# Performance work log

Measured on AMD Instinct MI355X. Metric: run time of the kernel, lower is better.

The kernel has to match this reference:

```python
import jax, jax.numpy as jnp
import numpy as np


def setup_inputs() -> dict:
    key = jax.random.key(0)
    k0, k1, k2, k3, k4 = jax.random.split(key, 5)
    B, C, H, W = 32, 64, 128, 128
    return {
        "x": jax.random.normal(k0, (B, C, H, W), jnp.float32),
        "w1d": jax.random.normal(k1, (64,), jnp.float32) * 0.1,   # Conv1d(1,1,k=64,s=64) weight
        "b1d": jax.random.normal(k2, (1,), jnp.float32) * 0.1,    # Conv1d bias
        "wdw": jax.random.normal(k3, (C, 1, 9, 9), jnp.float32) * 0.05,  # depthwise Conv2d weight (OIHW, groups=C)
        "bdw": jax.random.normal(k4, (C,), jnp.float32) * 0.05,   # depthwise Conv2d bias
    }


def _cov_linear(x, w1d, b1d):
    # Batched torch.cov over channels, followed by Conv1d(1,1,k=64,stride=64)
    B, C, H, W = x.shape
    f = x.reshape(B, C, H * W)
    f = f - f.mean(axis=-1, keepdims=True)
    cov = jnp.einsum('bcn,bdn->bcd', f, f) / (H * W - 1)  # [B, C, C]
    # Conv1d with kernel=stride=64 on the flattened C*C vector == segmented dot
    seg = cov.reshape(B, (C * C) // 64, 64)               # [B, C, 64] since C == 64
    return seg @ w1d + b1d                                # [B, C]


def reference(x, w1d, b1d, wdw, bdw):
    C = x.shape[1]
    c = _cov_linear(x, w1d, b1d)
    # 9x9 depthwise conv, padding=4 (same spatial size)
    y = jax.lax.conv_general_dilated(
        x, wdw, window_strides=(1, 1), padding=[(4, 4), (4, 4)],
        dimension_numbers=('NCHW', 'OIHW', 'NCHW'), feature_group_count=C)
    y = y + bdw[None, :, None, None]
    c_ = _cov_linear(y, w1d, b1d)
    raise_ch = jax.nn.softmax(c_ - c, axis=1)             # softmax over channel scores
    att = jax.nn.sigmoid(c_ * (1.0 + raise_ch))           # [B, C]
    return y * att[:, :, None, None]
```

## Files before the change

kernel.cpp:

```cpp
#include <hip/hip_runtime.h>

#define NSP 16384
#define CCH 64
#define BATCH 32
#define SPLIT 4
#define CPB (CCH / SPLIT)

#define LW 160
#define LH 40
#define LDSF (LW * LH)
#define NQ (LDSF / 4)
#define NISS 7

__device__ __forceinline__ void gload_lds16(const float* g, float* l) {
    __builtin_amdgcn_global_load_lds(
        (const __attribute__((address_space(1))) void*)g,
        (__attribute__((address_space(3))) void*)l,
        16, 0, 0);
}

__device__ __forceinline__ int swq(int q) { return q ^ ((q >> 3) & 7); }

__device__ __forceinline__ unsigned short f2bf(float f) {
    unsigned u = __float_as_uint(f);
    u += 0x7fffu + ((u >> 16) & 1u);
    return (unsigned short)(u >> 16);
}
__device__ __forceinline__ float bflo(unsigned u) { return __uint_as_float(u << 16); }
__device__ __forceinline__ float bfhi(unsigned u) { return __uint_as_float(u & 0xffff0000u); }

template<int YBF>
__global__ __launch_bounds__(256, 2) void conv_kernel(
    const float* __restrict__ x, const float* __restrict__ wdw,
    const float* __restrict__ bdw, const float* __restrict__ w1d,
    const float* __restrict__ zpad,
    float* __restrict__ yf, unsigned short* __restrict__ yb,
    float* __restrict__ tx_parts, float* __restrict__ ty_parts,
    float* __restrict__ S_x, float* __restrict__ S_y)
{
    const int tile = blockIdx.x;
    const int b    = blockIdx.y;
    const int sp   = blockIdx.z;
    const int tile_ry = tile * 32;
    const int tid = threadIdx.x;
    const int tx = tid & 15, ty = tid >> 4;
    const int c0 = tx * 8, r0 = ty * 2;
    const int cbase = sp * CPB;

    __shared__ float bufs[2][LDSF];

    int soff[NISS]; unsigned okm = 0;
    #pragma unroll
    for (int r = 0; r < NISS; ++r) {
        int q = tid + 256 * r;
        int lrow = q / 40, qcl = q - lrow * 40;
        int gq = swq(qcl);
        int gr = tile_ry - 4 + lrow;
        int gc = gq * 4 - 4;
        soff[r] = gr * 128 + gc;
        if (q < NQ && (unsigned)gr < 128u && gq >= 1 && gq <= 32) okm |= 1u << r;
    }

    int rb[4];
    #pragma unroll
    for (int j = 0; j < 4; ++j) rb[j] = r0 * LW + swq(2 * tx + j) * 4;

    const float* xb = x + (size_t)b * CCH * NSP;

#define STAGE(cc, dst) do {                                               \
        const float* plane_ = xb + (size_t)(cc) * NSP;                    \
        _Pragma("unroll")                                                 \
        for (int r_ = 0; r_ < NISS; ++r_) {                               \
            int q_ = tid + 256 * r_;                                      \
            if (q_ < NQ) {                                                \
                const float* g_ = ((okm >> r_) & 1u) ? plane_ + soff[r_]  \
                                                     : zpad;              \
                gload_lds16(g_, &(dst)[4 * q_]);                          \
            }                                                             \
        }                                                                 \
    } while (0)

    STAGE(cbase, bufs[0]);

    float txa[2][8] = {};
    float tya[2][8] = {};
    __syncthreads();

    for (int k = 0; k < CPB; ++k) {
        const int c = cbase + k;
        if (k + 1 < CPB) STAGE(c + 1, bufs[(k + 1) & 1]);

        const float* cb = bufs[k & 1];
        const float* wc = wdw + c * 81;
        float acc[2][8] = {};
        float cx[2][8];
        #pragma unroll
        for (int ir = 0; ir < 10; ++ir) {
            float4 f0 = *(const float4*)(cb + rb[0] + ir * LW);
            float4 f1 = *(const float4*)(cb + rb[1] + ir * LW);
            float4 f2 = *(const float4*)(cb + rb[2] + ir * LW);
            float4 f3 = *(const float4*)(cb + rb[3] + ir * LW);
            float v[16] = {f0.x, f0.y, f0.z, f0.w, f1.x, f1.y, f1.z, f1.w,
                           f2.x, f2.y, f2.z, f2.w, f3.x, f3.y, f3.z, f3.w};
            if (ir == 4) {
                #pragma unroll
                for (int q = 0; q < 8; ++q) cx[0][q] = v[q + 4];
            }
            if (ir == 5) {
                #pragma unroll
                for (int q = 0; q < 8; ++q) cx[1][q] = v[q + 4];
            }
            #pragma unroll
            for (int o = 0; o < 2; ++o) {
                int tv = ir - o;
                if (tv >= 0 && tv <= 8) {
                    #pragma unroll
                    for (int kx = 0; kx < 9; ++kx) {
                        float w = wc[tv * 9 + kx];
                        #pragma unroll
                        for (int q = 0; q < 8; ++q) acc[o][q] += w * v[kx + q];
                    }
                }
            }
        }

        const float bias = bdw[c];
        const float w1c  = w1d[c];
        float sx = 0.f, sy = 0.f;
        const size_t ybase = (size_t)(b * CCH + c) * NSP + (tile_ry + r0) * 128 + c0;
        #pragma unroll
        for (int o = 0; o < 2; ++o) {
            float yv[8];
            #pragma unroll
            for (int q = 0; q < 8; ++q) {
                yv[q] = acc[o][q] + bias;
                sx += cx[o][q];
                sy += yv[q];
                txa[o][q] += w1c * cx[o][q];
                tya[o][q] += w1c * yv[q];
            }
            if (YBF) {
                uint4 s;
                s.x = (unsigned)f2bf(yv[0]) | ((unsigned)f2bf(yv[1]) << 16);
                s.y = (unsigned)f2bf(yv[2]) | ((unsigned)f2bf(yv[3]) << 16);
                s.z = (unsigned)f2bf(yv[4]) | ((unsigned)f2bf(yv[5]) << 16);
                s.w = (unsigned)f2bf(yv[6]) | ((unsigned)f2bf(yv[7]) << 16);
                *(uint4*)(yb + ybase + o * 128) = s;
            } else {
                *(float4*)(yf + ybase + o * 128) =
                    make_float4(yv[0], yv[1], yv[2], yv[3]);
                *(float4*)(yf + ybase + o * 128 + 4) =
                    make_float4(yv[4], yv[5], yv[6], yv[7]);
            }
        }

        #pragma unroll
        for (int off = 32; off > 0; off >>= 1) {
            sx += __shfl_down(sx, off);
            sy += __shfl_down(sy, off);
        }
        if ((tid & 63) == 0) {
            atomicAdd(&S_x[b * CCH + c], sx);
            atomicAdd(&S_y[b * CCH + c], sy);
        }
        __syncthreads();
    }
#undef STAGE

    const size_t tb = ((size_t)sp * BATCH + b) * NSP + (tile_ry + r0) * 128 + c0;
    float* txp = tx_parts + tb;
    float* typ = ty_parts + tb;
    #pragma unroll
    for (int o = 0; o < 2; ++o) {
        *(float4*)(txp + o * 128)     = make_float4(txa[o][0], txa[o][1], txa[o][2], txa[o][3]);
        *(float4*)(txp + o * 128 + 4) = make_float4(txa[o][4], txa[o][5], txa[o][6], txa[o][7]);
        *(float4*)(typ + o * 128)     = make_float4(tya[o][0], tya[o][1], tya[o][2], tya[o][3]);
        *(float4*)(typ + o * 128 + 4) = make_float4(tya[o][4], tya[o][5], tya[o][6], tya[o][7]);
    }
}

__global__ __launch_bounds__(256) void collapse_kernel(
    const float4* __restrict__ parts, float4* __restrict__ tcoll)
{
    const int i = blockIdx.x * 256 + threadIdx.x;
    const int tsel = i >> 17;
    const int j = i & 131071;
    const float4* p = parts + (size_t)tsel * SPLIT * 131072;
    float4 s = p[j];
    #pragma unroll
    for (int r = 1; r < SPLIT; ++r) {
        float4 a = p[j + (size_t)r * 131072];
        s.x += a.x; s.y += a.y; s.z += a.z; s.w += a.w;
    }
    tcoll[(size_t)tsel * 131072 + j] = s;
}

template<int YBF>
__global__ __launch_bounds__(256) void dot_kernel(
    const float* __restrict__ x, const float* __restrict__ yf,
    const unsigned short* __restrict__ yb,
    const float* __restrict__ t_x, const float* __restrict__ t_y,
    float* __restrict__ dot_x, float* __restrict__ dot_y)
{
    const int bc = blockIdx.x;
    const int b  = bc >> 6;
    const int tid = threadIdx.x;
    const float4* xr  = (const float4*)(x   + (size_t)bc * NSP);
    const float4* txr = (const float4*)(t_x + (size_t)b * NSP);
    const float4* tyr = (const float4*)(t_y + (size_t)b * NSP);
    float dx = 0.f, dy = 0.f;
    if (YBF) {
        const uint4* yr = (const uint4*)(yb + (size_t)bc * NSP);
        for (int i = tid; i < NSP / 8; i += 256) {
            float4 x0 = xr[2 * i], x1 = xr[2 * i + 1];
            float4 t0 = txr[2 * i], t1 = txr[2 * i + 1];
            float4 u0 = tyr[2 * i], u1 = tyr[2 * i + 1];
            uint4 yv = yr[i];
            dx += x0.x * t0.x + x0.y * t0.y + x0.z * t0.z + x0.w * t0.w
                + x1.x * t1.x + x1.y * t1.y + x1.z * t1.z + x1.w * t1.w;
            dy += bflo(yv.x) * u0.x + bfhi(yv.x) * u0.y
                + bflo(yv.y) * u0.z + bfhi(yv.y) * u0.w
                + bflo(yv.z) * u1.x + bfhi(yv.z) * u1.y
                + bflo(yv.w) * u1.z + bfhi(yv.w) * u1.w;
        }
    } else {
        const float4* yr = (const float4*)(yf + (size_t)bc * NSP);
        for (int i = tid; i < NSP / 4; i += 256) {
            float4 xv = xr[i], tv = txr[i];
            float4 yv = yr[i], uv = tyr[i];
            dx += xv.x * tv.x + xv.y * tv.y + xv.z * tv.z + xv.w * tv.w;
            dy += yv.x * uv.x + yv.y * uv.y + yv.z * uv.z + yv.w * uv.w;
        }
    }
    #pragma unroll
    for (int off = 32; off > 0; off >>= 1) {
        dx += __shfl_down(dx, off);
        dy += __shfl_down(dy, off);
    }
    __shared__ float red[8];
    const int wid = tid >> 6;
    if ((tid & 63) == 0) { red[wid * 2] = dx; red[wid * 2 + 1] = dy; }
    __syncthreads();
    if (tid == 0) {
        dot_x[bc] = red[0] + red[2] + red[4] + red[6];
        dot_y[bc] = red[1] + red[3] + red[5] + red[7];
    }
}

__global__ __launch_bounds__(64) void att_kernel(
    const float* __restrict__ S_x, const float* __restrict__ S_y,
    const float* __restrict__ dot_x, const float* __restrict__ dot_y,
    const float* __restrict__ w1d, const float* __restrict__ b1d,
    float* __restrict__ att)
{
    const int b = blockIdx.x;
    const int c = threadIdx.x;
    const float sx = S_x[b * CCH + c];
    const float sy = S_y[b * CCH + c];
    const float w  = w1d[c];
    float tsx = w * sx, tsy = w * sy;
    #pragma unroll
    for (int off = 32; off > 0; off >>= 1) {
        tsx += __shfl_xor(tsx, off);
        tsy += __shfl_xor(tsy, off);
    }
    const float inv_n  = 1.f / 16384.f;
    const float inv_n1 = 1.f / 16383.f;
    const float bb = b1d[0];
    float cxv = (dot_x[b * CCH + c] - sx * inv_n * tsx) * inv_n1 + bb;
    float cyv = (dot_y[b * CCH + c] - sy * inv_n * tsy) * inv_n1 + bb;
    float d = cyv - cxv;
    float m = d;
    #pragma unroll
    for (int off = 32; off > 0; off >>= 1) m = fmaxf(m, __shfl_xor(m, off));
    float e = __expf(d - m);
    float s = e;
    #pragma unroll
    for (int off = 32; off > 0; off >>= 1) s += __shfl_xor(s, off);
    float r = e / s;
    float a = cyv * (1.f + r);
    att[b * CCH + c] = 1.f / (1.f + __expf(-a));
}

template<int YBF>
__global__ __launch_bounds__(256) void scale_kernel(
    const unsigned short* __restrict__ yb, float* __restrict__ out,
    const float* __restrict__ att)
{
    const size_t total8 = (size_t)BATCH * CCH * NSP / 8;
    size_t i = (size_t)blockIdx.x * blockDim.x + threadIdx.x;
    const size_t stride = (size_t)gridDim.x * blockDim.x;
    if (YBF) {
        for (; i < total8; i += stride) {
            uint4 y = ((const uint4*)yb)[i];
            float a = att[(i * 8) >> 14];
            float4 o0 = make_float4(bflo(y.x) * a, bfhi(y.x) * a,
                                    bflo(y.y) * a, bfhi(y.y) * a);
            float4 o1 = make_float4(bflo(y.z) * a, bfhi(y.z) * a,
                                    bflo(y.w) * a, bfhi(y.w) * a);
            ((float4*)out)[2 * i]     = o0;
            ((float4*)out)[2 * i + 1] = o1;
        }
    } else {
        for (; i < total8; i += stride) {
            float a = att[(i * 8) >> 14];
            float4 v0 = ((const float4*)out)[2 * i];
            float4 v1 = ((const float4*)out)[2 * i + 1];
            v0.x *= a; v0.y *= a; v0.z *= a; v0.w *= a;
            v1.x *= a; v1.y *= a; v1.z *= a; v1.w *= a;
            ((float4*)out)[2 * i]     = v0;
            ((float4*)out)[2 * i + 1] = v1;
        }
    }
}

extern "C" void kernel_launch(void* const* d_in, const int* in_sizes, int n_in,
                              void* d_out, int out_size, void* d_ws, size_t ws_size,
                              hipStream_t stream) {
    const float* x   = (const float*)d_in[0];
    const float* w1d = (const float*)d_in[1];
    const float* b1d = (const float*)d_in[2];
    const float* wdw = (const float*)d_in[3];
    const float* bdw = (const float*)d_in[4];
    float* out = (float*)d_out;
    float* fw  = (float*)d_ws;

    const size_t PARTS = (size_t)SPLIT * BATCH * NSP;
    float* tx_parts = fw;
    float* ty_parts = tx_parts + PARTS;
    float* t_x      = ty_parts + PARTS;
    float* t_y      = t_x + (size_t)BATCH * NSP;
    float* S_x      = t_y + (size_t)BATCH * NSP;
    float* S_y      = S_x + 2048;
    float* dot_x    = S_y + 2048;
    float* dot_y    = dot_x + 2048;
    float* att      = dot_y + 2048;
    float* zpad     = att + 2048;
    float* fend     = zpad + 64;
    size_t fbytes   = (size_t)((char*)fend - (char*)fw);
    fbytes = (fbytes + 255) & ~(size_t)255;
    unsigned short* yb = (unsigned short*)((char*)d_ws + fbytes);
    const size_t yb_bytes = (size_t)BATCH * CCH * NSP * 2;

    const bool ybf = (ws_size >= fbytes + yb_bytes);

    hipMemsetAsync(S_x, 0, 2 * 2048 * sizeof(float), stream);
    hipMemsetAsync(zpad, 0, 64 * sizeof(float), stream);

    if (ybf) {
        conv_kernel<1><<<dim3(4, BATCH, SPLIT), 256, 0, stream>>>(
            x, wdw, bdw, w1d, zpad, out, yb, tx_parts, ty_parts, S_x, S_y);
        collapse_kernel<<<1024, 256, 0, stream>>>((const float4*)tx_parts, (float4*)t_x);
        dot_kernel<1><<<2048, 256, 0, stream>>>(x, out, yb, t_x, t_y, dot_x, dot_y);
        att_kernel<<<BATCH, 64, 0, stream>>>(S_x, S_y, dot_x, dot_y, w1d, b1d, att);
        scale_kernel<1><<<2048, 256, 0, stream>>>(yb, out, att);
    } else {
        conv_kernel<0><<<dim3(4, BATCH, SPLIT), 256, 0, stream>>>(
            x, wdw, bdw, w1d, zpad, out, yb, tx_parts, ty_parts, S_x, S_y);
        collapse_kernel<<<1024, 256, 0, stream>>>((const float4*)tx_parts, (float4*)t_x);
        dot_kernel<0><<<2048, 256, 0, stream>>>(x, out, yb, t_x, t_y, dot_x, dot_y);
        att_kernel<<<BATCH, 64, 0, stream>>>(S_x, S_y, dot_x, dot_y, w1d, b1d, att);
        scale_kernel<0><<<2048, 256, 0, stream>>>(yb, out, att);
    }
}
```

Baseline: 180.9 us.

## Load depthwise conv halo directly from global memory instead of LDS staging

Removes the double-buffered LDS staging (global_load_lds with swizzle) and the per-channel barrier in the depthwise conv kernel. Each thread now reads its 10 rows of float4 halo data straight from global memory, relying on L1/L2 caches for the reuse between neighbouring threads. This drops the LDS footprint and the synchronisation, which may raise occupancy. In exchange there are more global/cache transactions and no explicit prefetch overlap.

```diff
diff --git a/kernel.cpp b/kernel.cpp
--- a/kernel.cpp
+++ b/kernel.cpp
@@ -5,21 +5,6 @@
 #define BATCH 32
 #define SPLIT 4
 #define CPB (CCH / SPLIT)
-
-#define LW 160
-#define LH 40
-#define LDSF (LW * LH)
-#define NQ (LDSF / 4)
-#define NISS 7
-
-__device__ __forceinline__ void gload_lds16(const float* g, float* l) {
-    __builtin_amdgcn_global_load_lds(
-        (const __attribute__((address_space(1))) void*)g,
-        (__attribute__((address_space(3))) void*)l,
-        16, 0, 0);
-}
-
-__device__ __forceinline__ int swq(int q) { return q ^ ((q >> 3) & 7); }
 
 __device__ __forceinline__ unsigned short f2bf(float f) {
     unsigned u = __float_as_uint(f);
@@ -47,59 +32,33 @@
     const int c0 = tx * 8, r0 = ty * 2;
     const int cbase = sp * CPB;
 
-    __shared__ float bufs[2][LDSF];
-
-    int soff[NISS]; unsigned okm = 0;
-    #pragma unroll
-    for (int r = 0; r < NISS; ++r) {
-        int q = tid + 256 * r;
-        int lrow = q / 40, qcl = q - lrow * 40;
-        int gq = swq(qcl);
-        int gr = tile_ry - 4 + lrow;
-        int gc = gq * 4 - 4;
-        soff[r] = gr * 128 + gc;
-        if (q < NQ && (unsigned)gr < 128u && gq >= 1 && gq <= 32) okm |= 1u << r;
-    }
-
-    int rb[4];
-    #pragma unroll
-    for (int j = 0; j < 4; ++j) rb[j] = r0 * LW + swq(2 * tx + j) * 4;
+    const bool e0 = (tx > 0);
+    const bool e3 = (tx < 15);
 
     const float* xb = x + (size_t)b * CCH * NSP;
-
-#define STAGE(cc, dst) do {                                               \
-        const float* plane_ = xb + (size_t)(cc) * NSP;                    \
-        _Pragma("unroll")                                                 \
-        for (int r_ = 0; r_ < NISS; ++r_) {                               \
-            int q_ = tid + 256 * r_;                                      \
-            if (q_ < NQ) {                                                \
-                const float* g_ = ((okm >> r_) & 1u) ? plane_ + soff[r_]  \
-                                                     : zpad;              \
-                gload_lds16(g_, &(dst)[4 * q_]);                          \
-            }                                                             \
-        }                                                                 \
-    } while (0)
-
-    STAGE(cbase, bufs[0]);
 
     float txa[2][8] = {};
     float tya[2][8] = {};
-    __syncthreads();
 
     for (int k = 0; k < CPB; ++k) {
         const int c = cbase + k;
-        if (k + 1 < CPB) STAGE(c + 1, bufs[(k + 1) & 1]);
-
-        const float* cb = bufs[k & 1];
+        const float* plane = xb + (size_t)c * NSP;
         const float* wc = wdw + c * 81;
         float acc[2][8] = {};
         float cx[2][8];
         #pragma unroll
         for (int ir = 0; ir < 10; ++ir) {
-            float4 f0 = *(const float4*)(cb + rb[0] + ir * LW);
-            float4 f1 = *(const float4*)(cb + rb[1] + ir * LW);
-            float4 f2 = *(const float4*)(cb + rb[2] + ir * LW);
-            float4 f3 = *(const float4*)(cb + rb[3] + ir * LW);
+            const int gr = tile_ry + r0 + ir - 4;
+            const bool rok = ((unsigned)gr < 128u);
+            const float* base = plane + gr * 128 + (c0 - 4);
+            const float* p0 = (rok && e0) ? base      : zpad;
+            const float* p1 = rok         ? base + 4  : zpad;
+            const float* p2 = rok         ? base + 8  : zpad;
+            const float* p3 = (rok && e3) ? base + 12 : zpad;
+            float4 f0 = *(const float4*)p0;
+            float4 f1 = *(const float4*)p1;
+            float4 f2 = *(const float4*)p2;
+            float4 f3 = *(const float4*)p3;
             float v[16] = {f0.x, f0.y, f0.z, f0.w, f1.x, f1.y, f1.z, f1.w,
                            f2.x, f2.y, f2.z, f2.w, f3.x, f3.y, f3.z, f3.w};
             if (ir == 4) {
@@ -163,9 +122,7 @@
             atomicAdd(&S_x[b * CCH + c], sx);
             atomicAdd(&S_y[b * CCH + c], sy);
         }
-        __syncthreads();
-    }
-#undef STAGE
+    }
 
     const size_t tb = ((size_t)sp * BATCH + b) * NSP + (tile_ry + r0) * 128 + c0;
     float* txp = tx_parts + tb;
```

Measured after the change: 202.2 us. 11.8% more time.

## Move x-side reductions out of conv kernel and double the channel split

Applied to the files above, without the earlier changes.

The conv kernel no longer accumulates the x-side weighted sum, per-channel sums or atomics. A new tcomp kernel computes t_x directly from x and sums the y partials. The per-channel sums move into the dot kernel, which already streams x and y. SPLIT rises to 8 with 3 blocks per SM for more conv parallelism, at the cost of reading x again and summing more partial buffers.

```diff
diff --git a/kernel.cpp b/kernel.cpp
--- a/kernel.cpp
+++ b/kernel.cpp
@@ -3,7 +3,7 @@
 #define NSP 16384
 #define CCH 64
 #define BATCH 32
-#define SPLIT 4
+#define SPLIT 8
 #define CPB (CCH / SPLIT)
 
 #define LW 160
@@ -30,13 +30,12 @@
 __device__ __forceinline__ float bfhi(unsigned u) { return __uint_as_float(u & 0xffff0000u); }
 
 template<int YBF>
-__global__ __launch_bounds__(256, 2) void conv_kernel(
+__global__ __launch_bounds__(256, 3) void conv_kernel(
     const float* __restrict__ x, const float* __restrict__ wdw,
     const float* __restrict__ bdw, const float* __restrict__ w1d,
     const float* __restrict__ zpad,
     float* __restrict__ yf, unsigned short* __restrict__ yb,
-    float* __restrict__ tx_parts, float* __restrict__ ty_parts,
-    float* __restrict__ S_x, float* __restrict__ S_y)
+    float* __restrict__ ty_parts)
 {
     const int tile = blockIdx.x;
     const int b    = blockIdx.y;
@@ -82,7 +81,6 @@
 
     STAGE(cbase, bufs[0]);
 
-    float txa[2][8] = {};
     float tya[2][8] = {};
     __syncthreads();
 
@@ -93,7 +91,6 @@
         const float* cb = bufs[k & 1];
         const float* wc = wdw + c * 81;
         float acc[2][8] = {};
-        float cx[2][8];
         #pragma unroll
         for (int ir = 0; ir < 10; ++ir) {
             float4 f0 = *(const float4*)(cb + rb[0] + ir * LW);
@@ -102,14 +99,6 @@
             float4 f3 = *(const float4*)(cb + rb[3] + ir * LW);
             float v[16] = {f0.x, f0.y, f0.z, f0.w, f1.x, f1.y, f1.z, f1.w,
                            f2.x, f2.y, f2.z, f2.w, f3.x, f3.y, f3.z, f3.w};
-            if (ir == 4) {
-                #pragma unroll
-                for (int q = 0; q < 8; ++q) cx[0][q] = v[q + 4];
-            }
-            if (ir == 5) {
-                #pragma unroll
-                for (int q = 0; q < 8; ++q) cx[1][q] = v[q + 4];
-            }
             #pragma unroll
             for (int o = 0; o < 2; ++o) {
                 int tv = ir - o;
@@ -126,7 +115,6 @@
 
         const float bias = bdw[c];
         const float w1c  = w1d[c];
-        float sx = 0.f, sy = 0.f;
         const size_t ybase = (size_t)(b * CCH + c) * NSP + (tile_ry + r0) * 128 + c0;
         #pragma unroll
         for (int o = 0; o < 2; ++o) {
@@ -134,9 +122,6 @@
             #pragma unroll
             for (int q = 0; q < 8; ++q) {
                 yv[q] = acc[o][q] + bias;
-                sx += cx[o][q];
-                sy += yv[q];
-                txa[o][q] += w1c * cx[o][q];
                 tya[o][q] += w1c * yv[q];
             }
             if (YBF) {
@@ -153,46 +138,43 @@
                     make_float4(yv[4], yv[5], yv[6], yv[7]);
             }
         }
-
-        #pragma unroll
-        for (int off = 32; off > 0; off >>= 1) {
-            sx += __shfl_down(sx, off);
-            sy += __shfl_down(sy, off);
-        }
-        if ((tid & 63) == 0) {
-            atomicAdd(&S_x[b * CCH + c], sx);
-            atomicAdd(&S_y[b * CCH + c], sy);
-        }
         __syncthreads();
     }
 #undef STAGE
 
     const size_t tb = ((size_t)sp * BATCH + b) * NSP + (tile_ry + r0) * 128 + c0;
-    float* txp = tx_parts + tb;
     float* typ = ty_parts + tb;
     #pragma unroll
     for (int o = 0; o < 2; ++o) {
-        *(float4*)(txp + o * 128)     = make_float4(txa[o][0], txa[o][1], txa[o][2], txa[o][3]);
-        *(float4*)(txp + o * 128 + 4) = make_float4(txa[o][4], txa[o][5], txa[o][6], txa[o][7]);
         *(float4*)(typ + o * 128)     = make_float4(tya[o][0], tya[o][1], tya[o][2], tya[o][3]);
         *(float4*)(typ + o * 128 + 4) = make_float4(tya[o][4], tya[o][5], tya[o][6], tya[o][7]);
     }
 }
 
-__global__ __launch_bounds__(256) void collapse_kernel(
-    const float4* __restrict__ parts, float4* __restrict__ tcoll)
-{
-    const int i = blockIdx.x * 256 + threadIdx.x;
-    const int tsel = i >> 17;
-    const int j = i & 131071;
-    const float4* p = parts + (size_t)tsel * SPLIT * 131072;
-    float4 s = p[j];
-    #pragma unroll
-    for (int r = 1; r < SPLIT; ++r) {
-        float4 a = p[j + (size_t)r * 131072];
-        s.x += a.x; s.y += a.y; s.z += a.z; s.w += a.w;
-    }
-    tcoll[(size_t)tsel * 131072 + j] = s;
+__global__ __launch_bounds__(256) void tcomp_kernel(
+    const float4* __restrict__ x4, const float4* __restrict__ parts,
+    const float* __restrict__ w1d,
+    float4* __restrict__ t_x, float4* __restrict__ t_y)
+{
+    const int b = blockIdx.y;
+    const int p = blockIdx.x * 256 + threadIdx.x;
+    const float4* xb = x4 + (size_t)b * CCH * (NSP / 4) + p;
+    float4 ax = make_float4(0.f, 0.f, 0.f, 0.f);
+    #pragma unroll 8
+    for (int c = 0; c < CCH; ++c) {
+        float w = w1d[c];
+        float4 v = xb[(size_t)c * (NSP / 4)];
+        ax.x += w * v.x; ax.y += w * v.y; ax.z += w * v.z; ax.w += w * v.w;
+    }
+    float4 ay = make_float4(0.f, 0.f, 0.f, 0.f);
+    const float4* pb = parts + (size_t)b * (NSP / 4) + p;
+    #pragma unroll
+    for (int r = 0; r < SPLIT; ++r) {
+        float4 v = pb[(size_t)r * BATCH * (NSP / 4)];
+        ay.x += v.x; ay.y += v.y; ay.z += v.z; ay.w += v.w;
+    }
+    t_x[(size_t)b * (NSP / 4) + p] = ax;
+    t_y[(size_t)b * (NSP / 4) + p] = ay;
 }
 
 template<int YBF>
@@ -200,7 +182,8 @@
     const float* __restrict__ x, const float* __restrict__ yf,
     const unsigned short* __restrict__ yb,
     const float* __restrict__ t_x, const float* __restrict__ t_y,
-    float* __restrict__ dot_x, float* __restrict__ dot_y)
+    float* __restrict__ dot_x, float* __restrict__ dot_y,
+    float* __restrict__ S_x, float* __restrict__ S_y)
 {
     const int bc = blockIdx.x;
     const int b  = bc >> 6;
@@ -208,7 +191,7 @@
     const float4* xr  = (const float4*)(x   + (size_t)bc * NSP);
     const float4* txr = (const float4*)(t_x + (size_t)b * NSP);
     const float4* tyr = (const float4*)(t_y + (size_t)b * NSP);
-    float dx = 0.f, dy = 0.f;
+    float dx = 0.f, dy = 0.f, sx = 0.f, sy = 0.f;
     if (YBF) {
         const uint4* yr = (const uint4*)(yb + (size_t)bc * NSP);
         for (int i = tid; i < NSP / 8; i += 256) {
@@ -216,12 +199,14 @@
             float4 t0 = txr[2 * i], t1 = txr[2 * i + 1];
             float4 u0 = tyr[2 * i], u1 = tyr[2 * i + 1];
             uint4 yv = yr[i];
+            float y0 = bflo(yv.x), y1 = bfhi(yv.x), y2 = bflo(yv.y), y3 = bfhi(yv.y);
+            float y4 = bflo(yv.z), y5 = bfhi(yv.z), y6 = bflo(yv.w), y7 = bfhi(yv.w);
             dx += x0.x * t0.x + x0.y * t0.y + x0.z * t0.z + x0.w * t0.w
                 + x1.x * t1.x + x1.y * t1.y + x1.z * t1.z + x1.w * t1.w;
-            dy += bflo(yv.x) * u0.x + bfhi(yv.x) * u0.y
-                + bflo(yv.y) * u0.z + bfhi(yv.y) * u0.w
-                + bflo(yv.z) * u1.x + bfhi(yv.z) * u1.y
-                + bflo(yv.w) * u1.z + bfhi(yv.w) * u1.w;
+            sx += x0.x + x0.y + x0.z + x0.w + x1.x + x1.y + x1.z + x1.w;
+            dy += y0 * u0.x + y1 * u0.y + y2 * u0.z + y3 * u0.w
+                + y4 * u1.x + y5 * u1.y + y6 * u1.z + y7 * u1.w;
+            sy += y0 + y1 + y2 + y3 + y4 + y5 + y6 + y7;
         }
     } else {
         const float4* yr = (const float4*)(yf + (size_t)bc * NSP);
@@ -229,21 +214,30 @@
             float4 xv = xr[i], tv = txr[i];
             float4 yv = yr[i], uv = tyr[i];
             dx += xv.x * tv.x + xv.y * tv.y + xv.z * tv.z + xv.w * tv.w;
+            sx += xv.x + xv.y + xv.z + xv.w;
             dy += yv.x * uv.x + yv.y * uv.y + yv.z * uv.z + yv.w * uv.w;
+            sy += yv.x + yv.y + yv.z + yv.w;
         }
     }
     #pragma unroll
     for (int off = 32; off > 0; off >>= 1) {
         dx += __shfl_down(dx, off);
         dy += __shfl_down(dy, off);
-    }
-    __shared__ float red[8];
+        sx += __shfl_down(sx, off);
+        sy += __shfl_down(sy, off);
+    }
+    __shared__ float red[16];
     const int wid = tid >> 6;
-    if ((tid & 63) == 0) { red[wid * 2] = dx; red[wid * 2 + 1] = dy; }
+    if ((tid & 63) == 0) {
+        red[wid * 4]     = dx; red[wid * 4 + 1] = dy;
+        red[wid * 4 + 2] = sx; red[wid * 4 + 3] = sy;
+    }
     __syncthreads();
     if (tid == 0) {
-        dot_x[bc] = red[0] + red[2] + red[4] + red[6];
-        dot_y[bc] = red[1] + red[3] + red[5] + red[7];
+        dot_x[bc] = red[0] + red[4] + red[8]  + red[12];
+        dot_y[bc] = red[1] + red[5] + red[9]  + red[13];
+        S_x[bc]   = red[2] + red[6] + red[10] + red[14];
+        S_y[bc]   = red[3] + red[7] + red[11] + red[15];
     }
 }
 
@@ -325,10 +319,9 @@
     float* out = (float*)d_out;
     float* fw  = (float*)d_ws;
 
-    const size_t PARTS = (size_t)SPLIT * BATCH * NSP;
-    float* tx_parts = fw;
-    float* ty_parts = tx_parts + PARTS;
-    float* t_x      = ty_parts + PARTS;
+    const size_t PARTSY = (size_t)SPLIT * BATCH * NSP;
+    float* ty_parts = fw;
+    float* t_x      = ty_parts + PARTSY;
     float* t_y      = t_x + (size_t)BATCH * NSP;
     float* S_x      = t_y + (size_t)BATCH * NSP;
     float* S_y      = S_x + 2048;
@@ -344,21 +337,26 @@
 
     const bool ybf = (ws_size >= fbytes + yb_bytes);
 
-    hipMemsetAsync(S_x, 0, 2 * 2048 * sizeof(float), stream);
     hipMemsetAsync(zpad, 0, 64 * sizeof(float), stream);
 
     if (ybf) {
         conv_kernel<1><<<dim3(4, BATCH, SPLIT), 256, 0, stream>>>(
-            x, wdw, bdw, w1d, zpad, out, yb, tx_parts, ty_parts, S_x, S_y);
-        collapse_kernel<<<1024, 256, 0, stream>>>((const float4*)tx_parts, (float4*)t_x);
-        dot_kernel<1><<<2048, 256, 0, stream>>>(x, out, yb, t_x, t_y, dot_x, dot_y);
+            x, wdw, bdw, w1d, zpad, out, yb, ty_parts);
+        tcomp_kernel<<<dim3(NSP / 4 / 256, BATCH), 256, 0, stream>>>(
+            (const float4*)x, (const float4*)ty_parts, w1d,
+            (float4*)t_x, (float4*)t_y);
+        dot_kernel<1><<<2048, 256, 0, stream>>>(x, out, yb, t_x, t_y,
+                                                dot_x, dot_y, S_x, S_y);
         att_kernel<<<BATCH, 64, 0, stream>>>(S_x, S_y, dot_x, dot_y, w1d, b1d, att);
         scale_kernel<1><<<2048, 256, 0, stream>>>(yb, out, att);
     } else {
         conv_kernel<0><<<dim3(4, BATCH, SPLIT), 256, 0, stream>>>(
-            x, wdw, bdw, w1d, zpad, out, yb, tx_parts, ty_parts, S_x, S_y);
-        collapse_kernel<<<1024, 256, 0, stream>>>((const float4*)tx_parts, (float4*)t_x);
-        dot_kernel<0><<<2048, 256, 0, stream>>>(x, out, yb, t_x, t_y, dot_x, dot_y);
+            x, wdw, bdw, w1d, zpad, out, yb, ty_parts);
+        tcomp_kernel<<<dim3(NSP / 4 / 256, BATCH), 256, 0, stream>>>(
+            (const float4*)x, (const float4*)ty_parts, w1d,
+            (float4*)t_x, (float4*)t_y);
+        dot_kernel<0><<<2048, 256, 0, stream>>>(x, out, yb, t_x, t_y,
+                                                dot_x, dot_y, S_x, S_y);
         att_kernel<<<BATCH, 64, 0, stream>>>(S_x, S_y, dot_x, dot_y, w1d, b1d, att);
         scale_kernel<0><<<2048, 256, 0, stream>>>(yb, out, att);
     }
```

Result: slower. 188.1 us (+4.0%).
